# Kernel optimization log

Hardware: AMD Instinct MI355X
Metric: run time of the kernel (lower is better)

The kernel has to match this reference:

```python
import jax, jax.numpy as jnp
import numpy as np

B, K, D, DK, DG, H = 4, 512, 768, 96, 96, 8  # batch, proposals, appearance, key, geo, n_relations


def setup_inputs() -> dict:
    key = jax.random.key(0)
    ks = jax.random.split(key, 12)
    s = 0.02
    return {
        "f_a": jax.random.normal(ks[0], (B, K, D), dtype=jnp.float32),
        "position_embedding": jax.random.uniform(ks[1], (B, K, K, DG), dtype=jnp.float32),
        "WG_w": jax.random.normal(ks[2], (H, DG), dtype=jnp.float32) * s,
        "WG_b": jnp.zeros((H,), dtype=jnp.float32),
        "WK_w": jax.random.normal(ks[3], (H, D, DK), dtype=jnp.float32) * s,
        "WK_b": jnp.zeros((H, DK), dtype=jnp.float32),
        "WQ_w": jax.random.normal(ks[4], (H, D, DK), dtype=jnp.float32) * s,
        "WQ_b": jnp.zeros((H, DK), dtype=jnp.float32),
        "WV_w": jax.random.normal(ks[5], (H, D, DK), dtype=jnp.float32) * s,
        "WV_b": jnp.zeros((H, DK), dtype=jnp.float32),
        "gamma": jnp.asarray(0.5, dtype=jnp.float32),
    }


def reference(f_a, position_embedding, WG_w, WG_b, WK_w, WK_b, WQ_w, WQ_b, WV_w, WV_b, gamma):
    dim_k = WK_w.shape[-1]
    # per-head projections: (B,K,D) x (H,D,DK) -> (B,H,K,DK)
    w_k = jnp.einsum('bkd,hdf->bhkf', f_a, WK_w) + WK_b[None, :, None, :]
    w_q = jnp.einsum('bkd,hdf->bhkf', f_a, WQ_w) + WQ_b[None, :, None, :]
    w_v = jnp.einsum('bkd,hdf->bhkf', f_a, WV_w) + WV_b[None, :, None, :]
    # scaled_dot[b,h,i,j] = <w_k[b,h,i], w_q[b,h,j]> / sqrt(dim_k)  (i: key row, j: query col)
    scores = jnp.einsum('bhif,bhjf->bhij', w_k, w_q) / np.sqrt(dim_k)
    # geometric gate: WG is Linear(DG, 1) per head, then ReLU -> (B,H,K,K)
    w_g = jax.nn.relu(jnp.einsum('bijg,hg->bhij', position_embedding, WG_w)
                      + WG_b[None, :, None, None])
    logits = jnp.log(jnp.clip(w_g, 1e-6, None)) + scores
    # torch Softmax(dim=1) over (B,K,K) = over the key index i -> axis 2 here
    attn = jax.nn.softmax(logits, axis=2)
    # output[b,j] = sum_i attn[b,h,i,j] * w_v[b,h,i,:]  -> (B,K,H,DK)
    out = jnp.einsum('bhij,bhif->bjhf', attn, w_v)
    b, k = f_a.shape[:2]
    concat = out.reshape(b, k, -1)  # concat over Nr heads, last dim = H*DK = D
    return gamma * concat + f_a
```

## Files before the change

kernel.cpp:

```cpp
#include <hip/hip_runtime.h>
#include <hip/hip_bf16.h>

#define B_ 4
#define K_ 512
#define D_ 768
#define DK_ 96
#define DG_ 96
#define H_ 8

typedef __attribute__((ext_vector_type(8))) __bf16 bf16x8;
typedef __attribute__((ext_vector_type(4))) float f32x4;

static __device__ __forceinline__ unsigned short f2bf(float x) {
  union { float f; unsigned int u; } v; v.f = x;
  unsigned int u = v.u;
  return (unsigned short)((u + 0x7FFFu + ((u >> 16) & 1u)) >> 16);
}

__global__ __launch_bounds__(256) void cast_fa_kernel(const float* __restrict__ fa,
                                                      unsigned short* __restrict__ fa16) {
  int t = blockIdx.x * 256 + threadIdx.x;
  float4 v = ((const float4*)fa)[t];
  ushort4 o;
  o.x = f2bf(v.x); o.y = f2bf(v.y); o.z = f2bf(v.z); o.w = f2bf(v.w);
  ((ushort4*)fa16)[t] = o;
}

__global__ __launch_bounds__(256) void prep_w_kernel(const float* __restrict__ wq,
                                                     const float* __restrict__ wk,
                                                     const float* __restrict__ wv,
                                                     unsigned short* __restrict__ wt16) {
  __shared__ unsigned short Ts[96][130];
  int bid = blockIdx.x;
  int dt = bid % 6; int rest = bid / 6;
  int h = rest % 8; int p = rest / 8;
  const float* w = (p == 0) ? wq : (p == 1) ? wk : wv;
  const float* src = w + ((size_t)h * D_ + dt * 128) * DK_;
  for (int c = threadIdx.x; c < 128 * 96; c += 256) {
    int dd = c / 96, f = c % 96;
    Ts[f][dd] = f2bf(src[c]);
  }
  __syncthreads();
  unsigned short* dst = wt16 + (size_t)(p * H_ + h) * DK_ * D_ + dt * 128;
  for (int c = threadIdx.x; c < 96 * 32; c += 256) {
    int f = c / 32, q = c % 32;
    ushort4 v;
    v.x = Ts[f][q * 4 + 0]; v.y = Ts[f][q * 4 + 1];
    v.z = Ts[f][q * 4 + 2]; v.w = Ts[f][q * 4 + 3];
    *(ushort4*)(dst + (size_t)f * D_ + q * 4) = v;
  }
}

__global__ __launch_bounds__(256) void proj_kernel(
    const unsigned short* __restrict__ fa16, const unsigned short* __restrict__ wt16,
    const float* __restrict__ bq, const float* __restrict__ bk, const float* __restrict__ bv,
    unsigned short* __restrict__ q16, unsigned short* __restrict__ k16,
    unsigned short* __restrict__ vt16) {
  __shared__ unsigned short Ts[96][130];
  int bid = blockIdx.x;
  int mt = bid & 3;  bid >>= 2;
  int b  = bid & 3;  bid >>= 2;
  int h  = bid & 7;  bid >>= 3;
  int p  = bid;
  int lane = threadIdx.x & 63, wid = threadIdx.x >> 6;
  int lr = lane & 15, lg = lane >> 4;
  int row0 = mt * 128 + wid * 32;

  const unsigned short* A  = fa16 + ((size_t)(b * K_ + row0)) * D_;
  const unsigned short* Bt = wt16 + ((size_t)(p * H_ + h)) * DK_ * D_;

  f32x4 acc[2][6];
#pragma unroll
  for (int i = 0; i < 2; i++)
#pragma unroll
    for (int c = 0; c < 6; c++) acc[i][c] = (f32x4){0.f, 0.f, 0.f, 0.f};

  auto LOADF = [&](bf16x8& a0, bf16x8& a1, bf16x8 (&bb)[6], int kk) {
    a0 = *(const bf16x8*)(A + (size_t)lr * D_ + kk * 32 + lg * 8);
    a1 = *(const bf16x8*)(A + (size_t)(16 + lr) * D_ + kk * 32 + lg * 8);
#pragma unroll
    for (int c = 0; c < 6; c++)
      bb[c] = *(const bf16x8*)(Bt + (size_t)(c * 16 + lr) * D_ + kk * 32 + lg * 8);
  };
  auto MF = [&](bf16x8& a0, bf16x8& a1, bf16x8 (&bb)[6]) {
#pragma unroll
    for (int c = 0; c < 6; c++) {
      acc[0][c] = __builtin_amdgcn_mfma_f32_16x16x32_bf16(a0, bb[c], acc[0][c], 0, 0, 0);
      acc[1][c] = __builtin_amdgcn_mfma_f32_16x16x32_bf16(a1, bb[c], acc[1][c], 0, 0, 0);
    }
  };

  bf16x8 a0X, a1X, bX[6], a0Y, a1Y, bY[6];
  LOADF(a0X, a1X, bX, 0);
  for (int kk = 0; kk < 24; kk += 2) {
    LOADF(a0Y, a1Y, bY, kk + 1);
    MF(a0X, a1X, bX);
    if (kk + 2 < 24) LOADF(a0X, a1X, bX, kk + 2);
    MF(a0Y, a1Y, bY);
  }

  const float* bias = (p == 0) ? bq : (p == 1) ? bk : bv;
  if (p == 2) {
#pragma unroll
    for (int i = 0; i < 2; i++)
#pragma unroll
      for (int c = 0; c < 6; c++) {
        int col = c * 16 + lr;
        float bb = bias[h * DK_ + col];
#pragma unroll
        for (int r = 0; r < 4; r++) {
          int lrow = wid * 32 + i * 16 + lg * 4 + r;
          Ts[col][lrow] = f2bf(acc[i][c][r] + bb);
        }
      }
    __syncthreads();
    unsigned short* dst = vt16 + (size_t)(b * H_ + h) * DK_ * K_ + mt * 128;
    for (int c2 = threadIdx.x; c2 < 96 * 32; c2 += 256) {
      int f = c2 / 32, q = c2 % 32;
      ushort4 v;
      v.x = Ts[f][q * 4 + 0]; v.y = Ts[f][q * 4 + 1];
      v.z = Ts[f][q * 4 + 2]; v.w = Ts[f][q * 4 + 3];
      *(ushort4*)(dst + (size_t)f * K_ + q * 4) = v;
    }
  } else {
    unsigned short* dst = (p == 0) ? q16 : k16;
#pragma unroll
    for (int i = 0; i < 2; i++)
#pragma unroll
      for (int c = 0; c < 6; c++) {
        int col = c * 16 + lr;
        float bb = bias[h * DK_ + col];
#pragma unroll
        for (int r = 0; r < 4; r++) {
          int row = row0 + i * 16 + lg * 4 + r;
          dst[((size_t)(b * H_ + h) * K_ + row) * DK_ + col] = f2bf(acc[i][c][r] + bb);
        }
      }
  }
}

__global__ __launch_bounds__(256) void scores_kernel(const unsigned short* __restrict__ q16,
                                                     const unsigned short* __restrict__ k16,
                                                     float* __restrict__ L) {
  int bid = blockIdx.x;
  int it = bid & 3;  bid >>= 2;
  int jt = bid & 3;  bid >>= 2;
  int h  = bid & 7;  bid >>= 3;
  int b  = bid;
  int lane = threadIdx.x & 63, wid = threadIdx.x >> 6;
  int lr = lane & 15, lg = lane >> 4;
  int j0 = jt * 128 + wid * 32;
  int i0 = it * 128;
  const unsigned short* Q  = q16 + ((size_t)(b * H_ + h) * K_ + j0) * DK_;
  const unsigned short* Kp = k16 + ((size_t)(b * H_ + h) * K_ + i0) * DK_;

  f32x4 acc[2][8];
#pragma unroll
  for (int x = 0; x < 2; x++)
#pragma unroll
    for (int c = 0; c < 8; c++) acc[x][c] = (f32x4){0.f, 0.f, 0.f, 0.f};

#pragma unroll
  for (int kk = 0; kk < 3; kk++) {
    bf16x8 a0 = *(const bf16x8*)(Q + (size_t)lr * DK_ + kk * 32 + lg * 8);
    bf16x8 a1 = *(const bf16x8*)(Q + (size_t)(16 + lr) * DK_ + kk * 32 + lg * 8);
#pragma unroll
    for (int c = 0; c < 8; c++) {
      bf16x8 bfr = *(const bf16x8*)(Kp + (size_t)(c * 16 + lr) * DK_ + kk * 32 + lg * 8);
      acc[0][c] = __builtin_amdgcn_mfma_f32_16x16x32_bf16(a0, bfr, acc[0][c], 0, 0, 0);
      acc[1][c] = __builtin_amdgcn_mfma_f32_16x16x32_bf16(a1, bfr, acc[1][c], 0, 0, 0);
    }
  }

  const float scale = 0.10206207261596577f;
  float* Lb = L + ((size_t)(b * H_ + h) * K_ + j0) * K_ + i0;
#pragma unroll
  for (int x = 0; x < 2; x++)
#pragma unroll
    for (int c = 0; c < 8; c++)
#pragma unroll
      for (int r = 0; r < 4; r++) {
        int jl = x * 16 + lg * 4 + r;
        int il = c * 16 + lr;
        Lb[(size_t)jl * K_ + il] = acc[x][c][r] * scale;
      }
}

#define GS_PAD 516
__global__ __launch_bounds__(512) void gatesm_kernel(
    const float* __restrict__ pe, const float* __restrict__ wgw,
    const float* __restrict__ wgb, const float* __restrict__ L,
    unsigned short* __restrict__ p16) {
  extern __shared__ float Ls[];
  int b = blockIdx.x >> 7;
  int j0 = (blockIdx.x & 127) * 4;
  int t = threadIdx.x;
  int wv = t >> 6, lane = t & 63;
  int lr3 = (lane >> 3) & 7;
  int lg3 = lane & 7;
  const float4* pe4 = (const float4*)pe;
  const float4* wg4 = (const float4*)wgw;

  for (int p = 0; p < 8; p++) {
    int i = wv * 64 + p * 8 + lr3;
    float4 pev[4][3];
#pragma unroll
    for (int j = 0; j < 4; j++) {
      size_t base = ((size_t)(b * K_ + i) * K_ + (j0 + j)) * (DG_ / 4);
#pragma unroll
      for (int c = 0; c < 3; c++) pev[j][c] = pe4[base + lg3 + 8 * c];
    }
#pragma unroll
    for (int h = 0; h < H_; h++) {
      float4 w0 = wg4[h * 24 + lg3];
      float4 w1 = wg4[h * 24 + lg3 + 8];
      float4 w2 = wg4[h * 24 + lg3 + 16];
      float bias = wgb[h];
      float acc[4];
#pragma unroll
      for (int j = 0; j < 4; j++) {
        acc[j] = pev[j][0].x * w0.x + pev[j][0].y * w0.y + pev[j][0].z * w0.z + pev[j][0].w * w0.w
               + pev[j][1].x * w1.x + pev[j][1].y * w1.y + pev[j][1].z * w1.z + pev[j][1].w * w1.w
               + pev[j][2].x * w2.x + pev[j][2].y * w2.y + pev[j][2].z * w2.z + pev[j][2].w * w2.w;
      }
#pragma unroll
      for (int j = 0; j < 4; j++) {
        acc[j] += __shfl_xor(acc[j], 1);
        acc[j] += __shfl_xor(acc[j], 2);
        acc[j] += __shfl_xor(acc[j], 4);
      }
      if (lg3 == h) {
#pragma unroll
        for (int j = 0; j < 4; j++) {
          float lgt = __logf(fmaxf(acc[j] + bias, 1e-6f));
          Ls[(h * 4 + j) * GS_PAD + i] = lgt;
        }
      }
    }
  }
  __syncthreads();

#pragma unroll
  for (int rr = 0; rr < 4; rr++) {
    int row = wv * 4 + rr;
    int h = row >> 2, j = row & 3;
    const float* Lr = &Ls[row * GS_PAD];
    const float* Lg = L + ((size_t)(b * H_ + h) * K_ + (j0 + j)) * K_;
    float4 g0 = *(const float4*)(Lr + lane * 4);
    float4 g1 = *(const float4*)(Lr + 256 + lane * 4);
    float4 s0 = *(const float4*)(Lg + lane * 4);
    float4 s1 = *(const float4*)(Lg + 256 + lane * 4);
    float l0 = g0.x + s0.x, l1 = g0.y + s0.y, l2 = g0.z + s0.z, l3 = g0.w + s0.w;
    float l4 = g1.x + s1.x, l5 = g1.y + s1.y, l6 = g1.z + s1.z, l7 = g1.w + s1.w;
    float m = fmaxf(fmaxf(fmaxf(l0, l1), fmaxf(l2, l3)),
                    fmaxf(fmaxf(l4, l5), fmaxf(l6, l7)));
#pragma unroll
    for (int o = 32; o > 0; o >>= 1) m = fmaxf(m, __shfl_xor(m, o));
    float e0 = __expf(l0 - m), e1 = __expf(l1 - m), e2 = __expf(l2 - m), e3 = __expf(l3 - m);
    float e4 = __expf(l4 - m), e5 = __expf(l5 - m), e6 = __expf(l6 - m), e7 = __expf(l7 - m);
    float s = ((e0 + e1) + (e2 + e3)) + ((e4 + e5) + (e6 + e7));
#pragma unroll
    for (int o = 32; o > 0; o >>= 1) s += __shfl_xor(s, o);
    float inv = 1.0f / s;
    ushort4 o0, o1;
    o0.x = f2bf(e0 * inv); o0.y = f2bf(e1 * inv); o0.z = f2bf(e2 * inv); o0.w = f2bf(e3 * inv);
    o1.x = f2bf(e4 * inv); o1.y = f2bf(e5 * inv); o1.z = f2bf(e6 * inv); o1.w = f2bf(e7 * inv);
    ushort4* dst = (ushort4*)(p16 + ((size_t)(b * H_ + h) * K_ + (j0 + j)) * K_);
    dst[lane] = o0;
    dst[lane + 64] = o1;
  }
}

__global__ __launch_bounds__(256) void pv_kernel(const unsigned short* __restrict__ p16,
                                                 const unsigned short* __restrict__ vt16,
                                                 const float* __restrict__ fa,
                                                 const float* __restrict__ gptr,
                                                 float* __restrict__ out) {
  int bid = blockIdx.x;
  int mt = bid & 7; bid >>= 3;
  int h  = bid & 7; bid >>= 3;
  int b  = bid;
  int lane = threadIdx.x & 63, wid = threadIdx.x >> 6;
  int lr = lane & 15, lg = lane >> 4;
  int bh = b * H_ + h;
  int row0 = mt * 64 + wid * 16;
  const unsigned short* A = p16 + ((size_t)bh * K_ + row0) * K_;
  const unsigned short* V = vt16 + (size_t)bh * DK_ * K_;

  f32x4 acc[6];
#pragma unroll
  for (int c = 0; c < 6; c++) acc[c] = (f32x4){0.f, 0.f, 0.f, 0.f};

  for (int kk = 0; kk < 16; kk++) {
    bf16x8 a = *(const bf16x8*)(A + (size_t)lr * K_ + kk * 32 + lg * 8);
#pragma unroll
    for (int c = 0; c < 6; c++) {
      bf16x8 bfr = *(const bf16x8*)(V + (size_t)(c * 16 + lr) * K_ + kk * 32 + lg * 8);
      acc[c] = __builtin_amdgcn_mfma_f32_16x16x32_bf16(a, bfr, acc[c], 0, 0, 0);
    }
  }

  float gamma = gptr[0];
#pragma unroll
  for (int c = 0; c < 6; c++) {
    int fcol = c * 16 + lr;
#pragma unroll
    for (int r = 0; r < 4; r++) {
      int j = row0 + lg * 4 + r;
      size_t oidx = ((size_t)(b * K_ + j)) * D_ + h * DK_ + fcol;
      out[oidx] = gamma * acc[c][r] + fa[oidx];
    }
  }
}

extern "C" void kernel_launch(void* const* d_in, const int* in_sizes, int n_in,
                              void* d_out, int out_size, void* d_ws, size_t ws_size,
                              hipStream_t stream) {
  (void)in_sizes; (void)n_in; (void)out_size; (void)ws_size;
  const float* fa   = (const float*)d_in[0];
  const float* pe   = (const float*)d_in[1];
  const float* wgw  = (const float*)d_in[2];
  const float* wgb  = (const float*)d_in[3];
  const float* wkw  = (const float*)d_in[4];
  const float* wkb  = (const float*)d_in[5];
  const float* wqw  = (const float*)d_in[6];
  const float* wqb  = (const float*)d_in[7];
  const float* wvw  = (const float*)d_in[8];
  const float* wvb  = (const float*)d_in[9];
  const float* gptr = (const float*)d_in[10];
  float* out = (float*)d_out;

  char* ws = (char*)d_ws;
  unsigned short* fa16 = (unsigned short*)ws; ws += (size_t)B_ * K_ * D_ * 2;
  unsigned short* wt16 = (unsigned short*)ws; ws += (size_t)3 * H_ * DK_ * D_ * 2;
  unsigned short* q16  = (unsigned short*)ws; ws += (size_t)B_ * H_ * K_ * DK_ * 2;
  unsigned short* k16  = (unsigned short*)ws; ws += (size_t)B_ * H_ * K_ * DK_ * 2;
  unsigned short* vt16 = (unsigned short*)ws; ws += (size_t)B_ * H_ * DK_ * K_ * 2;
  float* L             = (float*)ws;          ws += (size_t)B_ * H_ * K_ * K_ * 4;
  unsigned short* p16  = (unsigned short*)ws;

  const int lds_bytes = 32 * GS_PAD * 4;
  hipFuncSetAttribute((const void*)gatesm_kernel,
                      hipFuncAttributeMaxDynamicSharedMemorySize, lds_bytes);

  cast_fa_kernel<<<(B_ * K_ * D_ / 4) / 256, 256, 0, stream>>>(fa, fa16);
  prep_w_kernel<<<144, 256, 0, stream>>>(wqw, wkw, wvw, wt16);
  proj_kernel<<<3 * H_ * B_ * 4, 256, 0, stream>>>(fa16, wt16, wqb, wkb, wvb, q16, k16, vt16);
  scores_kernel<<<B_ * H_ * 4 * 4, 256, 0, stream>>>(q16, k16, L);
  gatesm_kernel<<<B_ * 128, 512, lds_bytes, stream>>>(pe, wgw, wgb, L, p16);
  pv_kernel<<<B_ * H_ * 8, 256, 0, stream>>>(p16, vt16, fa, gptr, out);
}
```

Measured before the change: 186.2 us.

## Stage projection GEMM tiles through LDS and remap blocks for weight reuse

The projection kernel now loads A (activation) and B (weight) tiles cooperatively into padded shared memory with register prefetch of the next K-slice, instead of each wave loading its fragments directly from global memory. The four waves now share one B tile rather than each fetching it separately. The block index mapping is also reordered so that consecutive blocks share the same head/projection weights, which should improve L2 reuse. The cost is two barriers per K-step and LDS traffic. This only affects the projection stage, which is a small part of the pipeline.

```diff
diff --git a/kernel.cpp b/kernel.cpp
--- a/kernel.cpp
+++ b/kernel.cpp
@@ -56,18 +56,19 @@
     const float* __restrict__ bq, const float* __restrict__ bk, const float* __restrict__ bv,
     unsigned short* __restrict__ q16, unsigned short* __restrict__ k16,
     unsigned short* __restrict__ vt16) {
-  __shared__ unsigned short Ts[96][130];
+  __shared__ alignas(16) unsigned short SM[128 * 72 + 96 * 72];
+  unsigned short* As = SM;
+  unsigned short* Bs = SM + 128 * 72;
   int bid = blockIdx.x;
-  int mt = bid & 3;  bid >>= 2;
-  int b  = bid & 3;  bid >>= 2;
-  int h  = bid & 7;  bid >>= 3;
-  int p  = bid;
-  int lane = threadIdx.x & 63, wid = threadIdx.x >> 6;
+  int mt = bid & 15, ph = bid >> 4;
+  int p = ph >> 3, h = ph & 7;
+  int b = mt >> 2;
+  int t = threadIdx.x;
+  int lane = t & 63, wid = t >> 6;
   int lr = lane & 15, lg = lane >> 4;
-  int row0 = mt * 128 + wid * 32;
-
-  const unsigned short* A  = fa16 + ((size_t)(b * K_ + row0)) * D_;
-  const unsigned short* Bt = wt16 + ((size_t)(p * H_ + h)) * DK_ * D_;
+
+  const unsigned short* A  = fa16 + (size_t)(mt * 128) * D_;
+  const unsigned short* Bt = wt16 + (size_t)ph * DK_ * D_;
 
   f32x4 acc[2][6];
 #pragma unroll
@@ -75,32 +76,55 @@
 #pragma unroll
     for (int c = 0; c < 6; c++) acc[i][c] = (f32x4){0.f, 0.f, 0.f, 0.f};
 
-  auto LOADF = [&](bf16x8& a0, bf16x8& a1, bf16x8 (&bb)[6], int kk) {
-    a0 = *(const bf16x8*)(A + (size_t)lr * D_ + kk * 32 + lg * 8);
-    a1 = *(const bf16x8*)(A + (size_t)(16 + lr) * D_ + kk * 32 + lg * 8);
-#pragma unroll
-    for (int c = 0; c < 6; c++)
-      bb[c] = *(const bf16x8*)(Bt + (size_t)(c * 16 + lr) * D_ + kk * 32 + lg * 8);
+  uint4 ra[4], rb[3];
+  auto GLOAD = [&](int kk) {
+#pragma unroll
+    for (int q = 0; q < 4; q++) {
+      int c = t + 256 * q;
+      ra[q] = *(const uint4*)(A + (size_t)(c >> 3) * D_ + kk * 64 + (c & 7) * 8);
+    }
+#pragma unroll
+    for (int q = 0; q < 3; q++) {
+      int c = t + 256 * q;
+      rb[q] = *(const uint4*)(Bt + (size_t)(c >> 3) * D_ + kk * 64 + (c & 7) * 8);
+    }
   };
-  auto MF = [&](bf16x8& a0, bf16x8& a1, bf16x8 (&bb)[6]) {
-#pragma unroll
-    for (int c = 0; c < 6; c++) {
-      acc[0][c] = __builtin_amdgcn_mfma_f32_16x16x32_bf16(a0, bb[c], acc[0][c], 0, 0, 0);
-      acc[1][c] = __builtin_amdgcn_mfma_f32_16x16x32_bf16(a1, bb[c], acc[1][c], 0, 0, 0);
+  auto SWRITE = [&]() {
+#pragma unroll
+    for (int q = 0; q < 4; q++) {
+      int c = t + 256 * q;
+      *(uint4*)&As[(c >> 3) * 72 + (c & 7) * 8] = ra[q];
+    }
+#pragma unroll
+    for (int q = 0; q < 3; q++) {
+      int c = t + 256 * q;
+      *(uint4*)&Bs[(c >> 3) * 72 + (c & 7) * 8] = rb[q];
     }
   };
 
-  bf16x8 a0X, a1X, bX[6], a0Y, a1Y, bY[6];
-  LOADF(a0X, a1X, bX, 0);
-  for (int kk = 0; kk < 24; kk += 2) {
-    LOADF(a0Y, a1Y, bY, kk + 1);
-    MF(a0X, a1X, bX);
-    if (kk + 2 < 24) LOADF(a0X, a1X, bX, kk + 2);
-    MF(a0Y, a1Y, bY);
+  GLOAD(0);
+  for (int ks = 0; ks < 12; ks++) {
+    __syncthreads();
+    SWRITE();
+    __syncthreads();
+    if (ks + 1 < 12) GLOAD(ks + 1);
+#pragma unroll
+    for (int kkk = 0; kkk < 2; kkk++) {
+      bf16x8 a0 = *(const bf16x8*)&As[(wid * 32 + lr) * 72 + kkk * 32 + lg * 8];
+      bf16x8 a1 = *(const bf16x8*)&As[(wid * 32 + 16 + lr) * 72 + kkk * 32 + lg * 8];
+#pragma unroll
+      for (int c = 0; c < 6; c++) {
+        bf16x8 bb = *(const bf16x8*)&Bs[(c * 16 + lr) * 72 + kkk * 32 + lg * 8];
+        acc[0][c] = __builtin_amdgcn_mfma_f32_16x16x32_bf16(a0, bb, acc[0][c], 0, 0, 0);
+        acc[1][c] = __builtin_amdgcn_mfma_f32_16x16x32_bf16(a1, bb, acc[1][c], 0, 0, 0);
+      }
+    }
   }
 
   const float* bias = (p == 0) ? bq : (p == 1) ? bk : bv;
   if (p == 2) {
+    __syncthreads();
+    unsigned short* Tp = SM;
 #pragma unroll
     for (int i = 0; i < 2; i++)
 #pragma unroll
@@ -110,16 +134,16 @@
 #pragma unroll
         for (int r = 0; r < 4; r++) {
           int lrow = wid * 32 + i * 16 + lg * 4 + r;
-          Ts[col][lrow] = f2bf(acc[i][c][r] + bb);
+          Tp[col * 130 + lrow] = f2bf(acc[i][c][r] + bb);
         }
       }
     __syncthreads();
-    unsigned short* dst = vt16 + (size_t)(b * H_ + h) * DK_ * K_ + mt * 128;
-    for (int c2 = threadIdx.x; c2 < 96 * 32; c2 += 256) {
+    unsigned short* dst = vt16 + (size_t)(b * H_ + h) * DK_ * K_ + (mt & 3) * 128;
+    for (int c2 = t; c2 < 96 * 32; c2 += 256) {
       int f = c2 / 32, q = c2 % 32;
       ushort4 v;
-      v.x = Ts[f][q * 4 + 0]; v.y = Ts[f][q * 4 + 1];
-      v.z = Ts[f][q * 4 + 2]; v.w = Ts[f][q * 4 + 3];
+      v.x = Tp[f * 130 + q * 4 + 0]; v.y = Tp[f * 130 + q * 4 + 1];
+      v.z = Tp[f * 130 + q * 4 + 2]; v.w = Tp[f * 130 + q * 4 + 3];
       *(ushort4*)(dst + (size_t)f * K_ + q * 4) = v;
     }
   } else {
@@ -132,7 +156,7 @@
         float bb = bias[h * DK_ + col];
 #pragma unroll
         for (int r = 0; r < 4; r++) {
-          int row = row0 + i * 16 + lg * 4 + r;
+          int row = (mt & 3) * 128 + wid * 32 + i * 16 + lg * 4 + r;
           dst[((size_t)(b * H_ + h) * K_ + row) * DK_ + col] = f2bf(acc[i][c][r] + bb);
         }
       }
@@ -345,7 +369,7 @@
 
   cast_fa_kernel<<<(B_ * K_ * D_ / 4) / 256, 256, 0, stream>>>(fa, fa16);
   prep_w_kernel<<<144, 256, 0, stream>>>(wqw, wkw, wvw, wt16);
-  proj_kernel<<<3 * H_ * B_ * 4, 256, 0, stream>>>(fa16, wt16, wqb, wkb, wvb, q16, k16, vt16);
+  proj_kernel<<<384, 256, 0, stream>>>(fa16, wt16, wqb, wkb, wvb, q16, k16, vt16);
   scores_kernel<<<B_ * H_ * 4 * 4, 256, 0, stream>>>(q16, k16, L);
   gatesm_kernel<<<B_ * 128, 512, lds_bytes, stream>>>(pe, wgw, wgb, L, p16);
   pv_kernel<<<B_ * H_ * 8, 256, 0, stream>>>(p16, vt16, fa, gptr, out);
```

Measured after the change: 195.0 us. 1.05x slower.
